# Performance work log

Hardware: AMD Instinct MI355X
Metric: run time of the kernel (lower is better)

The kernel has to match this reference:

```python
import jax, jax.numpy as jnp
import numpy as np


def _conv1x1(x, W, b):
    # x: (B, Ci, H, W), W: (Co, Ci), b: (Co,)
    return jnp.einsum('oi,bihw->bohw', W, x) + b[None, :, None, None]


def setup_inputs() -> dict:
    key = jax.random.key(0)
    ks = jax.random.split(key, 12)
    B, C, H, W = 4, 256, 64, 64
    d = C // 2
    prev_c = 512
    s = lambda k, shape, scale=0.05: (jax.random.normal(k, shape, dtype=jnp.float32) * scale)
    return {
        'source_enc_f': jax.random.normal(ks[0], (B, C, H, W), dtype=jnp.float32),
        'target_enc_f': jax.random.normal(ks[1], (B, C, H, W), dtype=jnp.float32),
        'prev_inp': jax.random.normal(ks[2], (B, prev_c, H // 2, W // 2), dtype=jnp.float32),
        'Wq': s(ks[3], (d, C)), 'bq': s(ks[4], (d,)),
        'Wk': s(ks[5], (d, C)), 'bk': s(ks[6], (d,)),
        'Wv': s(ks[7], (d, C)), 'bv': s(ks[8], (d,)),
        'Wp': s(ks[9], (C, d)), 'bp': s(ks[10], (C,)),
        'gamma': jnp.zeros((1,), dtype=jnp.float32) + 0.1,  # nonzero so attn path contributes
        'Wc': s(ks[11], (C, C + prev_c, 3, 3)),
        'bc': jnp.zeros((C,), dtype=jnp.float32),
    }


def reference(source_enc_f, target_enc_f, prev_inp, Wq, bq, Wk, bk, Wv, bv, Wp, bp, gamma, Wc, bc):
    B, C, H, W = source_enc_f.shape
    d = Wq.shape[0]
    HW = H * W

    # --- AttnMech ---
    q = _conv1x1(source_enc_f, Wq, bq)   # (B, d, H, W)
    k = _conv1x1(target_enc_f, Wk, bk)
    v = _conv1x1(target_enc_f, Wv, bv)

    kf = k.reshape(B, d, HW)             # (B, d, HW)
    qf = q.reshape(B, d, HW)             # (B, d, HW)
    # scores[b, i, j] = sum_c key[b, c, i] * query[b, c, j]; no 1/sqrt(d) scaling
    scores = jnp.einsum('bci,bcj->bij', kf, qf)       # (B, HW, HW)
    attn = jax.nn.softmax(scores, axis=1)             # softmax over key axis (torch dim=1)

    vf = v.transpose(0, 2, 3, 1).reshape(B, HW, d)    # (B, HW, d)
    out = jnp.einsum('bij,bjc->bic', attn, vf)        # (B, HW, d)
    out = out.reshape(B, H, W, d).transpose(0, 3, 1, 2)  # (B, d, H, W)
    out = _conv1x1(out, Wp, bp)                       # (B, C, H, W)
    x = target_enc_f + gamma[0] * out

    # --- upsample (nearest, scale 2) + concat ---
    prev = jnp.repeat(jnp.repeat(prev_inp, 2, axis=2), 2, axis=3)
    x = jnp.concatenate([x, prev], axis=1)            # (B, C+prev_c, H, W)

    # --- 3x3 conv, stride 1, pad 1 ---
    x = jax.lax.conv_general_dilated(
        x, Wc, window_strides=(1, 1), padding=((1, 1), (1, 1)),
        dimension_numbers=('NCHW', 'OIHW', 'NCHW'))
    x = x + bc[None, :, None, None]

    # --- InstanceNorm2d (affine=False, eps=1e-5, biased var over HW) ---
    mean = jnp.mean(x, axis=(2, 3), keepdims=True)
    var = jnp.mean(jnp.square(x - mean), axis=(2, 3), keepdims=True)
    x = (x - mean) * jax.lax.rsqrt(var + 1e-5)

    return jax.nn.relu(x)
```

## Files before the change

### kernel.cpp

```cpp
#include <hip/hip_runtime.h>
#include <hip/hip_bf16.h>

#define BB 4
#define CC 256
#define HW 4096
#define DD 128

typedef __attribute__((ext_vector_type(8))) short bf16x8;
typedef __attribute__((ext_vector_type(4))) short bf16x4;
typedef __attribute__((ext_vector_type(4))) float f32x4;
typedef __attribute__((ext_vector_type(4))) unsigned uint4v;

static __device__ __forceinline__ void ld4(float* dst, const float* src) {
  float4 t = *(const float4*)src;
  dst[0] = t.x; dst[1] = t.y; dst[2] = t.z; dst[3] = t.w;
}

static __device__ __forceinline__ short f2b(float f) {
  unsigned u = __float_as_uint(f);
  u += 0x7fffu + ((u >> 16) & 1u);
  return (short)(u >> 16);
}
static __device__ __forceinline__ unsigned pk2(float lo, float hi) {
  return (unsigned)(unsigned short)f2b(lo) | ((unsigned)(unsigned short)f2b(hi) << 16);
}

static __device__ __forceinline__ void gl16(const short* g, short* l) {
  __builtin_amdgcn_global_load_lds(
      (const __attribute__((address_space(1))) unsigned*)g,
      (__attribute__((address_space(3))) unsigned*)l, 16, 0, 0);
}

__global__ __launch_bounds__(256) void k_qkv_mfma(
    const float* __restrict__ src, const float* __restrict__ tgt,
    const float* __restrict__ Wq, const float* __restrict__ bq,
    const float* __restrict__ Wk, const float* __restrict__ bk,
    const float* __restrict__ Wv, const float* __restrict__ bv,
    short* __restrict__ qb, short* __restrict__ kb, short* __restrict__ vb)
{
  __shared__ __align__(16) short Wt[128 * 40];
  __shared__ __align__(16) short Xt[64 * 40];
  __shared__ __align__(16) short T[9216];
  const int tid = threadIdx.x;
  const int wv = tid >> 6;
  const int lane = tid & 63;
  const int t = lane & 15, q = lane >> 4;
  const int px0 = blockIdx.x * 64;
  const int which = blockIdx.y;
  const int b = blockIdx.z;
  const float* X    = (which == 0) ? src : tgt;
  const float* Wm   = (which == 0) ? Wq : (which == 1) ? Wk : Wv;
  const float* bias = (which == 0) ? bq : (which == 1) ? bk : bv;

  const f32x4 zf = {0.f, 0.f, 0.f, 0.f};
  f32x4 acc[2][4];
#pragma unroll
  for (int mt = 0; mt < 2; ++mt)
#pragma unroll
    for (int nt = 0; nt < 4; ++nt) acc[mt][nt] = zf;

  for (int kk = 0; kk < CC; kk += 32) {
    __syncthreads();
#pragma unroll
    for (int u = 0; u < 4; ++u) {
      int e = tid + (u << 8);
      int row = e >> 3, cq = (e & 7) * 4;
      float4 w4 = *(const float4*)&Wm[row * CC + kk + cq];
      unsigned* dst = (unsigned*)(Wt + row * 40 + cq);
      dst[0] = pk2(w4.x, w4.y);
      dst[1] = pk2(w4.z, w4.w);
    }
#pragma unroll
    for (int u = 0; u < 2; ++u) {
      int e = tid + (u << 8);
      int c = e >> 4, p4 = (e & 15) * 4;
      float4 xv = *(const float4*)&X[((size_t)b * CC + kk + c) * HW + px0 + p4];
      Xt[(p4 + 0) * 40 + c] = f2b(xv.x);
      Xt[(p4 + 1) * 40 + c] = f2b(xv.y);
      Xt[(p4 + 2) * 40 + c] = f2b(xv.z);
      Xt[(p4 + 3) * 40 + c] = f2b(xv.w);
    }
    __syncthreads();
    bf16x8 af[2], bfr[4];
#pragma unroll
    for (int mt = 0; mt < 2; ++mt)
      af[mt] = *(const bf16x8*)(Wt + (wv * 32 + mt * 16 + t) * 40 + q * 8);
#pragma unroll
    for (int nt = 0; nt < 4; ++nt)
      bfr[nt] = *(const bf16x8*)(Xt + (nt * 16 + t) * 40 + q * 8);
#pragma unroll
    for (int mt = 0; mt < 2; ++mt)
#pragma unroll
      for (int nt = 0; nt < 4; ++nt)
        acc[mt][nt] = __builtin_amdgcn_mfma_f32_16x16x32_bf16(
            af[mt], bfr[nt], acc[mt][nt], 0, 0, 0);
  }
  __syncthreads();
  if (which < 2) {
#pragma unroll
    for (int mt = 0; mt < 2; ++mt) {
      int chb = wv * 32 + mt * 16 + q * 4;
#pragma unroll
      for (int r = 0; r < 4; ++r) {
        float bv_ = bias[chb + r];
#pragma unroll
        for (int nt = 0; nt < 4; ++nt)
          T[(nt * 16 + t) * 136 + chb + r] = f2b(acc[mt][nt][r] + bv_);
      }
    }
    __syncthreads();
    short* out = (which == 0) ? qb : kb;
    int p = tid >> 2, cq = (tid & 3) * 32;
    short* gdst = out + ((size_t)b * HW + px0 + p) * DD + cq;
#pragma unroll
    for (int e2 = 0; e2 < 4; ++e2)
      *(uint4*)(gdst + e2 * 8) = *(const uint4*)(T + p * 136 + cq + e2 * 8);
  } else {
#pragma unroll
    for (int mt = 0; mt < 2; ++mt) {
      int chb = wv * 32 + mt * 16 + q * 4;
#pragma unroll
      for (int r = 0; r < 4; ++r) {
        float bv_ = bias[chb + r];
#pragma unroll
        for (int nt = 0; nt < 4; ++nt)
          T[(chb + r) * 72 + nt * 16 + t] = f2b(acc[mt][nt][r] + bv_);
      }
    }
    __syncthreads();
    int ch = tid >> 1, pq = (tid & 1) * 32;
    short* gdst = vb + ((size_t)b * DD + ch) * HW + px0 + pq;
#pragma unroll
    for (int e2 = 0; e2 < 4; ++e2)
      *(uint4*)(gdst + e2 * 8) = *(const uint4*)(T + ch * 72 + pq + e2 * 8);
  }
}

__global__ __launch_bounds__(256) void k_lsum2(
    const short* __restrict__ qb, const short* __restrict__ kb,
    float* __restrict__ rl)
{
  __shared__ float lred[4][64];
  const int tid = threadIdx.x;
  const int w = tid >> 6;
  const int lane = tid & 63;
  const int t = lane & 15, q = lane >> 4;
  const int j0 = blockIdx.x * 64;
  const int ibeg = blockIdx.y * 1024;
  const int b = blockIdx.z;
  const short* qbb = qb + (size_t)b * HW * DD;
  const short* kbb = kb + (size_t)b * HW * DD;

  bf16x8 Bq[4][4];
#pragma unroll
  for (int nt = 0; nt < 4; ++nt)
#pragma unroll
    for (int kk = 0; kk < 4; ++kk)
      Bq[nt][kk] = *(const bf16x8*)(qbb + (size_t)(j0 + nt * 16 + t) * DD + kk * 32 + q * 8);

  float racc[4] = {0.f, 0.f, 0.f, 0.f};
  const f32x4 zf = {0.f, 0.f, 0.f, 0.f};

  for (int i = ibeg + w * 16; i < ibeg + 1024; i += 64) {
    bf16x8 Ak[4];
#pragma unroll
    for (int kk = 0; kk < 4; ++kk)
      Ak[kk] = *(const bf16x8*)(kbb + (size_t)(i + t) * DD + kk * 32 + q * 8);
#pragma unroll
    for (int nt = 0; nt < 4; ++nt) {
      f32x4 d = zf;
#pragma unroll
      for (int kk = 0; kk < 4; ++kk)
        d = __builtin_amdgcn_mfma_f32_16x16x32_bf16(Ak[kk], Bq[nt][kk], d, 0, 0, 0);
      racc[nt] += __expf(d[0]) + __expf(d[1]) + __expf(d[2]) + __expf(d[3]);
    }
  }
#pragma unroll
  for (int nt = 0; nt < 4; ++nt) {
    float r = racc[nt];
    r += __shfl_xor(r, 16);
    r += __shfl_xor(r, 32);
    if (q == 0) lred[w][nt * 16 + t] = r;
  }
  __syncthreads();
  if (tid < 64) {
    float sum = lred[0][tid] + lred[1][tid] + lred[2][tid] + lred[3][tid];
    atomicAdd(&rl[(size_t)b * HW + j0 + tid], sum);
  }
}

__global__ __launch_bounds__(256) void k_vs(
    const short* __restrict__ vb, const float* __restrict__ rl,
    short* __restrict__ vs)
{
  int id4 = (blockIdx.x * 256 + threadIdx.x) * 4;
  int j = id4 & (HW - 1);
  int b = id4 >> 19;
  uint2 pv = *(const uint2*)(vb + id4);
  float f0 = __uint_as_float(pv.x << 16);
  float f1 = __uint_as_float(pv.x & 0xffff0000u);
  float f2 = __uint_as_float(pv.y << 16);
  float f3 = __uint_as_float(pv.y & 0xffff0000u);
  const float* rlb = rl + (size_t)b * HW + j;
  unsigned u0 = pk2(f0 / rlb[0], f1 / rlb[1]);
  unsigned u1 = pk2(f2 / rlb[2], f3 / rlb[3]);
  *(uint2*)(vs + id4) = make_uint2(u0, u1);
}

__global__ __launch_bounds__(256, 2) void k_attn2(
    const short* __restrict__ qb, const short* __restrict__ kb,
    const short* __restrict__ vs, float* __restrict__ ao)
{
  __shared__ __align__(16) short Qs[2][64 * 136];
  __shared__ __align__(16) short Vp[2][128 * 72];
  const int tid = threadIdx.x;
  const int w = tid >> 6;
  const int lane = tid & 63;
  const int t = lane & 15, q = lane >> 4;
  const int b = blockIdx.z;
  const int i0 = blockIdx.x * 64 + w * 16;
  const int jbeg = blockIdx.y * 2048, jend = jbeg + 2048;
  const short* qbb = qb + (size_t)b * HW * DD;
  const short* kbb = kb + (size_t)b * HW * DD;
  const short* vsb = vs + (size_t)b * DD * HW;
  const f32x4 zf = {0.f, 0.f, 0.f, 0.f};

  bf16x8 Ak[4];
#pragma unroll
  for (int kk = 0; kk < 4; ++kk)
    Ak[kk] = *(const bf16x8*)(kbb + (size_t)(i0 + t) * DD + kk * 32 + q * 8);

  f32x4 acc[8];
#pragma unroll
  for (int nt = 0; nt < 8; ++nt) acc[nt] = zf;

  bf16x8 rq[4], rv[4];
#define LOADT(jt)                                                             \
  {                                                                           \
    _Pragma("unroll")                                                         \
    for (int r = 0; r < 4; ++r) {                                             \
      int e = tid + (r << 8);                                                 \
      rq[r] = *(const bf16x8*)(qbb + (size_t)((jt) + (e >> 4)) * DD +         \
                               (e & 15) * 8);                                 \
      rv[r] = *(const bf16x8*)(vsb + (size_t)(e >> 3) * HW + (jt) +           \
                               (e & 7) * 8);                                  \
    }                                                                         \
  }
#define WRITET(buf)                                                           \
  {                                                                           \
    _Pragma("unroll")                                                         \
    for (int r = 0; r < 4; ++r) {                                             \
      int e = tid + (r << 8);                                                 \
      *(bf16x8*)(Qs[buf] + (e >> 4) * 136 + (e & 15) * 8) = rq[r];            \
    }                                                                         \
    _Pragma("unroll")                                                         \
    for (int r = 0; r < 4; ++r) {                                             \
      int e = tid + (r << 8);                                                 \
      int c = e >> 3, u8 = e & 7;                                             \
      int kap = (u8 >> 2) * 32 + (u8 & 1) * 16 + ((u8 >> 1) & 1) * 4;         \
      bf16x4 lo = __builtin_shufflevector(rv[r], rv[r], 0, 1, 2, 3);          \
      bf16x4 hi = __builtin_shufflevector(rv[r], rv[r], 4, 5, 6, 7);          \
      *(bf16x4*)(Vp[buf] + c * 72 + kap) = lo;                                \
      *(bf16x4*)(Vp[buf] + c * 72 + kap + 8) = hi;                            \
    }                                                                         \
  }

  LOADT(jbeg);
  WRITET(0);
  LOADT(jbeg + 64);

  int cur = 0;
  for (int j = jbeg; j < jend; j += 64) {
    __syncthreads();
    if (j + 64 < jend) {
      WRITET(cur ^ 1);
      if (j + 128 < jend) LOADT(j + 128);
    }
    const short* Qb = Qs[cur];
    const short* Vb = Vp[cur];
    f32x4 sv[4];
#pragma unroll
    for (int nt = 0; nt < 4; ++nt) sv[nt] = zf;
#pragma unroll
    for (int nt = 0; nt < 4; ++nt)
#pragma unroll
      for (int kk = 0; kk < 4; ++kk) {
        bf16x8 bq = *(const bf16x8*)(Qb + (nt * 16 + t) * 136 + kk * 32 + q * 8);
        sv[nt] = __builtin_amdgcn_mfma_f32_16x16x32_bf16(bq, Ak[kk], sv[nt], 0, 0, 0);
      }
    bf16x8 ap[2];
#pragma unroll
    for (int ks = 0; ks < 2; ++ks) {
      unsigned w0 = pk2(__expf(sv[2 * ks][0]), __expf(sv[2 * ks][1]));
      unsigned w1 = pk2(__expf(sv[2 * ks][2]), __expf(sv[2 * ks][3]));
      unsigned w2 = pk2(__expf(sv[2 * ks + 1][0]), __expf(sv[2 * ks + 1][1]));
      unsigned w3 = pk2(__expf(sv[2 * ks + 1][2]), __expf(sv[2 * ks + 1][3]));
      uint4v pw = {w0, w1, w2, w3};
      ap[ks] = __builtin_bit_cast(bf16x8, pw);
    }
#pragma unroll
    for (int nt = 0; nt < 8; ++nt)
#pragma unroll
      for (int ks = 0; ks < 2; ++ks) {
        bf16x8 bv = *(const bf16x8*)(Vb + (nt * 16 + t) * 72 + ks * 32 + q * 8);
        acc[nt] = __builtin_amdgcn_mfma_f32_16x16x32_bf16(ap[ks], bv, acc[nt], 0, 0, 0);
      }
    cur ^= 1;
  }
#undef LOADT
#undef WRITET
  float* aob = ao + (size_t)b * DD * HW;
#pragma unroll
  for (int nt = 0; nt < 8; ++nt)
#pragma unroll
    for (int r = 0; r < 4; ++r)
      atomicAdd(&aob[(size_t)(nt * 16 + t) * HW + i0 + q * 4 + r], acc[nt][r]);
}

__global__ __launch_bounds__(256) void k_proj(
    const float* __restrict__ ao, const float* __restrict__ tgt,
    const float* __restrict__ Wp, const float* __restrict__ bp,
    const float* __restrict__ gamma, short* __restrict__ Xn)
{
  __shared__ float Wt[32][132];
  __shared__ float Xs[32][68];
  __shared__ float T[64][133];
  const int tid = threadIdx.x;
  const int tx = tid & 15, ty = tid >> 4;
  const int p0 = blockIdx.x * 64;
  const int ro = blockIdx.y * 128;
  const int b = blockIdx.z;
  const float g0 = gamma[0];

  float acc[8][4];
#pragma unroll
  for (int i = 0; i < 8; ++i)
#pragma unroll
    for (int j = 0; j < 4; ++j) acc[i][j] = 0.f;

  for (int kk = 0; kk < DD; kk += 32) {
    __syncthreads();
#pragma unroll
    for (int u = 0; u < 4; ++u) {
      int e = tid + 256 * u;
      int c4 = (e & 7) * 4, r = e >> 3;
      float w[4]; ld4(w, &Wp[(ro + r) * DD + kk + c4]);
      Wt[c4 + 0][r] = w[0]; Wt[c4 + 1][r] = w[1];
      Wt[c4 + 2][r] = w[2]; Wt[c4 + 3][r] = w[3];
    }
#pragma unroll
    for (int u = 0; u < 2; ++u) {
      int e = tid + 256 * u;
      int p4 = (e & 15) * 4, c = e >> 4;
      *(float4*)&Xs[c][p4] = *(const float4*)&ao[(b * DD + kk + c) * HW + p0 + p4];
    }
    __syncthreads();
#pragma unroll 4
    for (int c = 0; c < 32; ++c) {
      float wa[8], xb[4];
      ld4(wa, &Wt[c][ty * 8]); ld4(wa + 4, &Wt[c][ty * 8 + 4]);
      ld4(xb, &Xs[c][tx * 4]);
#pragma unroll
      for (int rr = 0; rr < 8; ++rr)
#pragma unroll
        for (int pp = 0; pp < 4; ++pp) acc[rr][pp] += wa[rr] * xb[pp];
    }
  }
#pragma unroll
  for (int rr = 0; rr < 8; ++rr) {
    int r = ro + ty * 8 + rr;
    int idx = (b * CC + r) * HW + p0 + tx * 4;
    float4 t4 = *(const float4*)&tgt[idx];
    float bpv = bp[r];
    T[tx * 4 + 0][ty * 8 + rr] = t4.x + g0 * (acc[rr][0] + bpv);
    T[tx * 4 + 1][ty * 8 + rr] = t4.y + g0 * (acc[rr][1] + bpv);
    T[tx * 4 + 2][ty * 8 + rr] = t4.z + g0 * (acc[rr][2] + bpv);
    T[tx * 4 + 3][ty * 8 + rr] = t4.w + g0 * (acc[rr][3] + bpv);
  }
  __syncthreads();
  {
    int p = tid >> 2, cq = (tid & 3) * 32;
    int h = p0 >> 6;
    unsigned* dst = (unsigned*)(Xn + ((((size_t)b * 66 + h + 1) * 66) + 1 + p) * 768 + ro + cq);
#pragma unroll
    for (int e = 0; e < 16; ++e)
      dst[e] = pk2(T[p][cq + 2 * e], T[p][cq + 2 * e + 1]);
  }
}

__global__ __launch_bounds__(256) void k_pack(
    const float* __restrict__ prev, short* __restrict__ Xn)
{
  __shared__ float tile[64][65];
  const int tid = threadIdx.x;
  const int h = blockIdx.x;
  const int ci0 = blockIdx.y * 64;
  const int b = blockIdx.z;

  {
    int w = tid & 63, r = tid >> 6;
    for (int cs = r; cs < 64; cs += 4)
      tile[cs][w] = prev[((size_t)b * 512 + ci0 + cs) * 1024 + (h >> 1) * 32 + (w >> 1)];
  }
  __syncthreads();
  {
    int ci = tid & 63, wq = tid >> 6;
    for (int ws2 = wq; ws2 < 64; ws2 += 4)
      Xn[((((size_t)b * 66 + h + 1) * 66) + 1 + ws2) * 768 + 256 + ci0 + ci] = f2b(tile[ci][ws2]);
  }
}

__global__ __launch_bounds__(256) void k_wb(
    const float* __restrict__ Wc, short* __restrict__ Wb)
{
  int i = blockIdx.x * 256 + threadIdx.x;
  int o = i / 6912;
  int rem = i - o * 6912;
  int khw = rem / 768;
  int ci = rem - khw * 768;
  Wb[i] = f2b(Wc[(size_t)o * 6912 + ci * 9 + khw]);
}

__global__ __launch_bounds__(256, 2) void k_conv_mfma(
    const short* __restrict__ Xn,
    const short* __restrict__ Wb,
    const float* __restrict__ bcw,
    short* __restrict__ cb)
{
  __shared__ __align__(16) short Wl[384 * 64];
  __shared__ __align__(16) short Xl[66 * 64];
  const int tid = threadIdx.x;
  const int wv = tid >> 6;
  const int lane = tid & 63;
  const int t = lane & 15, q = lane >> 4;
  const int h = blockIdx.x;
  const int m0blk = blockIdx.y * 128;
  const int b = blockIdx.z;

  const f32x4 zf = {0.f, 0.f, 0.f, 0.f};
  f32x4 acc[2][4];
#pragma unroll
  for (int mt = 0; mt < 2; ++mt)
#pragma unroll
    for (int nt = 0; nt < 4; ++nt) acc[mt][nt] = zf;

  for (int kh = 0; kh < 3; ++kh) {
    const short* wsrc = Wb + (size_t)m0blk * 6912 + (kh * 3) * 768;
    const short* xsrc = Xn + ((size_t)b * 66 + h + kh) * 66 * 768;
    for (int ci0 = 0; ci0 < 768; ci0 += 64) {
#pragma unroll
      for (int r = 0; r < 12; ++r) {
        int e = tid + (r << 8);
        int g = e & 7, row = e >> 3;
        int kw = row >> 7, cout = row & 127;
        int gs = g ^ (row & 7);
        gl16(wsrc + (size_t)cout * 6912 + kw * 768 + ci0 + gs * 8, Wl + e * 8);
      }
#pragma unroll
      for (int r = 0; r < 3; ++r) {
        int e = tid + (r << 8);
        if (e < 528) {
          int g = e & 7, px = e >> 3;
          int gs = g ^ (px & 7);
          gl16(xsrc + (size_t)px * 768 + ci0 + gs * 8, Xl + e * 8);
        }
      }
      __syncthreads();
#pragma unroll
      for (int kw = 0; kw < 3; ++kw) {
        bf16x8 af[2][2], bfr[4][2];
#pragma unroll
        for (int kk = 0; kk < 2; ++kk) {
#pragma unroll
          for (int mt = 0; mt < 2; ++mt) {
            int row = kw * 128 + wv * 32 + mt * 16 + t;
            int g = (kk * 4 + q) ^ (row & 7);
            af[mt][kk] = *(const bf16x8*)(Wl + row * 64 + g * 8);
          }
#pragma unroll
          for (int nt = 0; nt < 4; ++nt) {
            int row = nt * 16 + t + kw;
            int g = (kk * 4 + q) ^ (row & 7);
            bfr[nt][kk] = *(const bf16x8*)(Xl + row * 64 + g * 8);
          }
        }
#pragma unroll
        for (int kk = 0; kk < 2; ++kk)
#pragma unroll
          for (int mt = 0; mt < 2; ++mt)
#pragma unroll
            for (int nt = 0; nt < 4; ++nt)
              acc[mt][nt] = __builtin_amdgcn_mfma_f32_16x16x32_bf16(
                  af[mt][kk], bfr[nt][kk], acc[mt][nt], 0, 0, 0);
      }
      __syncthreads();
    }
  }
#pragma unroll
  for (int mt = 0; mt < 2; ++mt) {
    int om = m0blk + wv * 32 + mt * 16 + q * 4;
#pragma unroll
    for (int r = 0; r < 4; ++r) {
      float bias = bcw[om + r];
      short* orow = cb + ((size_t)b * CC + om + r) * HW + h * 64;
#pragma unroll
      for (int nt = 0; nt < 4; ++nt)
        orow[nt * 16 + t] = f2b(acc[mt][nt][r] + bias);
    }
  }
}

__global__ __launch_bounds__(256) void k_inorm(
    const short* __restrict__ cb, float* __restrict__ out)
{
  __shared__ float buf[4096];
  __shared__ float red[8];
  const int tid = threadIdx.x;
  const int ch = blockIdx.x;
  const short* srcp = cb + (size_t)ch * HW;

  float s = 0.f, sq = 0.f;
#pragma unroll
  for (int u = 0; u < 2; ++u) {
    int sidx = u * 2048 + tid * 8;
    uint4 pk = *(const uint4*)(srcp + sidx);
    float f[8];
    f[0] = __uint_as_float(pk.x << 16); f[1] = __uint_as_float(pk.x & 0xffff0000u);
    f[2] = __uint_as_float(pk.y << 16); f[3] = __uint_as_float(pk.y & 0xffff0000u);
    f[4] = __uint_as_float(pk.z << 16); f[5] = __uint_as_float(pk.z & 0xffff0000u);
    f[6] = __uint_as_float(pk.w << 16); f[7] = __uint_as_float(pk.w & 0xffff0000u);
#pragma unroll
    for (int e = 0; e < 8; ++e) {
      buf[sidx + e] = f[e];
      s += f[e];
      sq += f[e] * f[e];
    }
  }
#pragma unroll
  for (int m = 32; m >= 1; m >>= 1) {
    s  += __shfl_xor(s, m, 64);
    sq += __shfl_xor(sq, m, 64);
  }
  if ((tid & 63) == 0) { red[tid >> 6] = s; red[4 + (tid >> 6)] = sq; }
  __syncthreads();
  if (tid == 0) {
    float S = red[0] + red[1] + red[2] + red[3];
    float Q = red[4] + red[5] + red[6] + red[7];
    float mean = S * (1.f / HW);
    float var = Q * (1.f / HW) - mean * mean;
    red[0] = mean;
    red[1] = rsqrtf(var + 1e-5f);
  }
  __syncthreads();
  const float mean = red[0], rs = red[1];
#pragma unroll
  for (int u = 0; u < 4; ++u) {
    int idx = u * 1024 + tid * 4;
    float4 v = *(const float4*)&buf[idx];
    float4 o4 = make_float4(fmaxf((v.x - mean) * rs, 0.f),
                            fmaxf((v.y - mean) * rs, 0.f),
                            fmaxf((v.z - mean) * rs, 0.f),
                            fmaxf((v.w - mean) * rs, 0.f));
    *(float4*)&out[(size_t)ch * HW + idx] = o4;
  }
}

extern "C" void kernel_launch(void* const* d_in, const int* in_sizes, int n_in,
                              void* d_out, int out_size, void* d_ws, size_t ws_size,
                              hipStream_t stream) {
  const float* src  = (const float*)d_in[0];
  const float* tgt  = (const float*)d_in[1];
  const float* prev = (const float*)d_in[2];
  const float* Wq = (const float*)d_in[3];  const float* bq = (const float*)d_in[4];
  const float* Wk = (const float*)d_in[5];  const float* bk = (const float*)d_in[6];
  const float* Wv = (const float*)d_in[7];  const float* bv = (const float*)d_in[8];
  const float* Wp = (const float*)d_in[9];  const float* bp = (const float*)d_in[10];
  const float* gamma = (const float*)d_in[11];
  const float* Wc = (const float*)d_in[12]; const float* bcw = (const float*)d_in[13];

  float* ws = (float*)d_ws;
  short* qb = (short*)ws;
  short* kb = (short*)(ws + 1048576);
  short* vb = (short*)(ws + 2097152);
  float* rl = ws + 3145728;
  short* vs = (short*)(ws + 3162112);
  short* Xn = (short*)ws;
  float* ao = ws + 6690816;
  short* cb = (short*)(ws + 6690816);
  short* Wb = (short*)(ws + 8787968);

  k_qkv_mfma<<<dim3(64, 3, BB), 256, 0, stream>>>(src, tgt, Wq, bq, Wk, bk, Wv, bv, qb, kb, vb);
  hipMemsetAsync(rl, 0, (size_t)BB * HW * 4, stream);
  k_lsum2<<<dim3(64, 4, BB), 256, 0, stream>>>(qb, kb, rl);
  k_vs   <<<dim3(2048),      256, 0, stream>>>(vb, rl, vs);
  hipMemsetAsync(ao, 0, (size_t)2097152 * 4, stream);
  k_attn2<<<dim3(64, 2, BB), 256, 0, stream>>>(qb, kb, vs, ao);
  hipMemsetAsync(Xn, 0, (size_t)BB * 66 * 66 * 768 * 2, stream);
  k_proj <<<dim3(64, 2, BB), 256, 0, stream>>>(ao, tgt, Wp, bp, gamma, Xn);
  k_pack <<<dim3(64, 8, BB), 256, 0, stream>>>(prev, Xn);
  k_wb   <<<dim3(6912),      256, 0, stream>>>(Wc, Wb);
  k_conv_mfma<<<dim3(64, 2, BB), 256, 0, stream>>>(Xn, Wb, bcw, cb);
  k_inorm<<<dim3(1024),      256, 0, stream>>>(cb, (float*)d_out);
}
```

Measured before the change: 372.7 us.

## Switch attention kernel to 32x32x16 MFMA with XOR-swizzled Q tile

Rewrites the attention-output kernel to use 32x32x16 bf16 MFMA instead of 16x16x32, giving each wave 32 query rows and 128 rows per block. The j-range is split into four chunks, and the grid changes to match. The Q shared tile drops its padding in favour of an XOR swizzle to avoid bank conflicts, and the V permutation is adjusted for the new operand layout. The output accumulator changes to a [HW][D] layout so the atomics coalesce along channels, and k_proj now reads it transposed. The larger MFMA tiles are meant to reduce LDS traffic per flop, at the cost of more accumulator registers and twice as many atomic partial sums.

Result: faster. 336.3 us (-9.8%).

```diff
diff --git a/kernel.cpp b/kernel.cpp
--- a/kernel.cpp
+++ b/kernel.cpp
@@ -9,6 +9,7 @@
 typedef __attribute__((ext_vector_type(8))) short bf16x8;
 typedef __attribute__((ext_vector_type(4))) short bf16x4;
 typedef __attribute__((ext_vector_type(4))) float f32x4;
+typedef __attribute__((ext_vector_type(16))) float f32x16;
 typedef __attribute__((ext_vector_type(4))) unsigned uint4v;
 
 static __device__ __forceinline__ void ld4(float* dst, const float* src) {
@@ -211,28 +212,29 @@
     const short* __restrict__ qb, const short* __restrict__ kb,
     const short* __restrict__ vs, float* __restrict__ ao)
 {
-  __shared__ __align__(16) short Qs[2][64 * 136];
+  __shared__ __align__(16) short Qs[2][64 * 128];
   __shared__ __align__(16) short Vp[2][128 * 72];
   const int tid = threadIdx.x;
   const int w = tid >> 6;
   const int lane = tid & 63;
-  const int t = lane & 15, q = lane >> 4;
+  const int l31 = lane & 31, h = lane >> 5;
   const int b = blockIdx.z;
-  const int i0 = blockIdx.x * 64 + w * 16;
-  const int jbeg = blockIdx.y * 2048, jend = jbeg + 2048;
+  const int i0w = blockIdx.x * 128 + w * 32;
+  const int jbeg = blockIdx.y * 1024, jend = jbeg + 1024;
   const short* qbb = qb + (size_t)b * HW * DD;
   const short* kbb = kb + (size_t)b * HW * DD;
   const short* vsb = vs + (size_t)b * DD * HW;
-  const f32x4 zf = {0.f, 0.f, 0.f, 0.f};
-
-  bf16x8 Ak[4];
-#pragma unroll
-  for (int kk = 0; kk < 4; ++kk)
-    Ak[kk] = *(const bf16x8*)(kbb + (size_t)(i0 + t) * DD + kk * 32 + q * 8);
-
-  f32x4 acc[8];
-#pragma unroll
-  for (int nt = 0; nt < 8; ++nt) acc[nt] = zf;
+
+  bf16x8 Bk[8];
+#pragma unroll
+  for (int kk = 0; kk < 8; ++kk)
+    Bk[kk] = *(const bf16x8*)(kbb + (size_t)(i0w + l31) * DD + kk * 16 + h * 8);
+
+  f32x16 acc[4];
+#pragma unroll
+  for (int nt = 0; nt < 4; ++nt)
+#pragma unroll
+    for (int e = 0; e < 16; ++e) acc[nt][e] = 0.f;
 
   bf16x8 rq[4], rv[4];
 #define LOADT(jt)                                                             \
@@ -251,13 +253,15 @@
     _Pragma("unroll")                                                         \
     for (int r = 0; r < 4; ++r) {                                             \
       int e = tid + (r << 8);                                                 \
-      *(bf16x8*)(Qs[buf] + (e >> 4) * 136 + (e & 15) * 8) = rq[r];            \
+      int row = e >> 4;                                                       \
+      int slot = (e & 15) ^ (row & 15);                                       \
+      *(bf16x8*)(Qs[buf] + row * 128 + slot * 8) = rq[r];                     \
     }                                                                         \
     _Pragma("unroll")                                                         \
     for (int r = 0; r < 4; ++r) {                                             \
       int e = tid + (r << 8);                                                 \
       int c = e >> 3, u8 = e & 7;                                             \
-      int kap = (u8 >> 2) * 32 + (u8 & 1) * 16 + ((u8 >> 1) & 1) * 4;         \
+      int kap = (u8 >> 2) * 32 + ((u8 >> 1) & 1) * 16 + (u8 & 1) * 4;         \
       bf16x4 lo = __builtin_shufflevector(rv[r], rv[r], 0, 1, 2, 3);          \
       bf16x4 hi = __builtin_shufflevector(rv[r], rv[r], 4, 5, 6, 7);          \
       *(bf16x4*)(Vp[buf] + c * 72 + kap) = lo;                                \
@@ -278,43 +282,50 @@
     }
     const short* Qb = Qs[cur];
     const short* Vb = Vp[cur];
-    f32x4 sv[4];
-#pragma unroll
-    for (int nt = 0; nt < 4; ++nt) sv[nt] = zf;
-#pragma unroll
-    for (int nt = 0; nt < 4; ++nt)
-#pragma unroll
-      for (int kk = 0; kk < 4; ++kk) {
-        bf16x8 bq = *(const bf16x8*)(Qb + (nt * 16 + t) * 136 + kk * 32 + q * 8);
-        sv[nt] = __builtin_amdgcn_mfma_f32_16x16x32_bf16(bq, Ak[kk], sv[nt], 0, 0, 0);
+    f32x16 sv[2];
+#pragma unroll
+    for (int ntj = 0; ntj < 2; ++ntj)
+#pragma unroll
+      for (int e = 0; e < 16; ++e) sv[ntj][e] = 0.f;
+#pragma unroll
+    for (int ntj = 0; ntj < 2; ++ntj)
+#pragma unroll
+      for (int kk = 0; kk < 8; ++kk) {
+        int row = ntj * 32 + l31;
+        int slot = (kk * 2 + h) ^ (row & 15);
+        bf16x8 aq = *(const bf16x8*)(Qb + row * 128 + slot * 8);
+        sv[ntj] = __builtin_amdgcn_mfma_f32_32x32x16_bf16(aq, Bk[kk], sv[ntj], 0, 0, 0);
       }
-    bf16x8 ap[2];
-#pragma unroll
-    for (int ks = 0; ks < 2; ++ks) {
-      unsigned w0 = pk2(__expf(sv[2 * ks][0]), __expf(sv[2 * ks][1]));
-      unsigned w1 = pk2(__expf(sv[2 * ks][2]), __expf(sv[2 * ks][3]));
-      unsigned w2 = pk2(__expf(sv[2 * ks + 1][0]), __expf(sv[2 * ks + 1][1]));
-      unsigned w3 = pk2(__expf(sv[2 * ks + 1][2]), __expf(sv[2 * ks + 1][3]));
+    bf16x8 ap[4];
+#pragma unroll
+    for (int s = 0; s < 4; ++s) {
+      const int tI = s >> 1, base = (s & 1) * 8;
+      unsigned w0 = pk2(__expf(sv[tI][base + 0]), __expf(sv[tI][base + 1]));
+      unsigned w1 = pk2(__expf(sv[tI][base + 2]), __expf(sv[tI][base + 3]));
+      unsigned w2 = pk2(__expf(sv[tI][base + 4]), __expf(sv[tI][base + 5]));
+      unsigned w3 = pk2(__expf(sv[tI][base + 6]), __expf(sv[tI][base + 7]));
       uint4v pw = {w0, w1, w2, w3};
-      ap[ks] = __builtin_bit_cast(bf16x8, pw);
-    }
-#pragma unroll
-    for (int nt = 0; nt < 8; ++nt)
-#pragma unroll
-      for (int ks = 0; ks < 2; ++ks) {
-        bf16x8 bv = *(const bf16x8*)(Vb + (nt * 16 + t) * 72 + ks * 32 + q * 8);
-        acc[nt] = __builtin_amdgcn_mfma_f32_16x16x32_bf16(ap[ks], bv, acc[nt], 0, 0, 0);
+      ap[s] = __builtin_bit_cast(bf16x8, pw);
+    }
+#pragma unroll
+    for (int ntc = 0; ntc < 4; ++ntc)
+#pragma unroll
+      for (int s = 0; s < 4; ++s) {
+        bf16x8 bv = *(const bf16x8*)(Vb + (ntc * 32 + l31) * 72 + s * 16 + h * 8);
+        acc[ntc] = __builtin_amdgcn_mfma_f32_32x32x16_bf16(ap[s], bv, acc[ntc], 0, 0, 0);
       }
     cur ^= 1;
   }
 #undef LOADT
 #undef WRITET
-  float* aob = ao + (size_t)b * DD * HW;
-#pragma unroll
-  for (int nt = 0; nt < 8; ++nt)
-#pragma unroll
-    for (int r = 0; r < 4; ++r)
-      atomicAdd(&aob[(size_t)(nt * 16 + t) * HW + i0 + q * 4 + r], acc[nt][r]);
+  float* aob = ao + (size_t)b * HW * DD;
+#pragma unroll
+  for (int ntc = 0; ntc < 4; ++ntc)
+#pragma unroll
+    for (int rg = 0; rg < 16; ++rg) {
+      int i = i0w + (rg & 3) + 8 * (rg >> 2) + 4 * h;
+      atomicAdd(&aob[(size_t)i * DD + ntc * 32 + l31], acc[ntc][rg]);
+    }
 }
 
 __global__ __launch_bounds__(256) void k_proj(
@@ -351,8 +362,10 @@
 #pragma unroll
     for (int u = 0; u < 2; ++u) {
       int e = tid + 256 * u;
-      int p4 = (e & 15) * 4, c = e >> 4;
-      *(float4*)&Xs[c][p4] = *(const float4*)&ao[(b * DD + kk + c) * HW + p0 + p4];
+      int p = e >> 3, c4 = (e & 7) * 4;
+      float4 v = *(const float4*)&ao[((size_t)b * HW + p0 + p) * DD + kk + c4];
+      Xs[c4 + 0][p] = v.x; Xs[c4 + 1][p] = v.y;
+      Xs[c4 + 2][p] = v.z; Xs[c4 + 3][p] = v.w;
     }
     __syncthreads();
 #pragma unroll 4
@@ -380,8 +393,8 @@
   __syncthreads();
   {
     int p = tid >> 2, cq = (tid & 3) * 32;
-    int h = p0 >> 6;
-    unsigned* dst = (unsigned*)(Xn + ((((size_t)b * 66 + h + 1) * 66) + 1 + p) * 768 + ro + cq);
+    int hh = p0 >> 6;
+    unsigned* dst = (unsigned*)(Xn + ((((size_t)b * 66 + hh + 1) * 66) + 1 + p) * 768 + ro + cq);
 #pragma unroll
     for (int e = 0; e < 16; ++e)
       dst[e] = pk2(T[p][cq + 2 * e], T[p][cq + 2 * e + 1]);
@@ -594,7 +607,7 @@
   k_lsum2<<<dim3(64, 4, BB), 256, 0, stream>>>(qb, kb, rl);
   k_vs   <<<dim3(2048),      256, 0, stream>>>(vb, rl, vs);
   hipMemsetAsync(ao, 0, (size_t)2097152 * 4, stream);
-  k_attn2<<<dim3(64, 2, BB), 256, 0, stream>>>(qb, kb, vs, ao);
+  k_attn2<<<dim3(32, 4, BB), 256, 0, stream>>>(qb, kb, vs, ao);
   hipMemsetAsync(Xn, 0, (size_t)BB * 66 * 66 * 768 * 2, stream);
   k_proj <<<dim3(64, 2, BB), 256, 0, stream>>>(ao, tgt, Wp, bp, gamma, Xn);
   k_pack <<<dim3(64, 8, BB), 256, 0, stream>>>(prev, Xn);
```
